# Kernel tuning notes

Measured on AMD Instinct MI355X. Metric: run time of the kernel, lower is better.

The kernel has to match this reference:

```python
import jax, jax.numpy as jnp
import numpy as np

B, N_VIS = 2, 512
T, HP, WP = 8, 16, 16
L = T * HP * WP              # 2048 tokens
D, HEAD_DIM = 384, 48
N_HEADS = D // HEAD_DIM      # 8
N_LAYERS, F_DIM = 8, 1536
EPS = 1e-6
THETA = 10000.0


def _rms(x, w):
    return x * jax.lax.rsqrt(jnp.mean(x * x, axis=-1, keepdims=True) + EPS) * w


def _rope_cos_sin(t, h, w):
    # VideoRotaryEmbeddingSplit466: split head_dim//2 freqs 4:6:6 over (t,h,w)
    half = HEAD_DIM // 2
    inv = 1.0 / (THETA ** (jnp.arange(half, dtype=jnp.float32) / half))
    dt = half * 4 // 16
    dh = half * 6 // 16
    l = jnp.arange(t * h * w)
    tp = l // (h * w)
    rem = l % (h * w)
    hp = rem // w
    wp = rem % w
    f = jnp.concatenate([tp[:, None] * inv[:dt],
                         hp[:, None] * inv[dt:dt + dh],
                         wp[:, None] * inv[dt + dh:]], axis=1)   # (L, half)
    emb = jnp.concatenate([f, f], axis=-1)                        # (L, HEAD_DIM)
    return jnp.cos(emb), jnp.sin(emb)


def _rot_half(x):
    x1, x2 = jnp.split(x, 2, axis=-1)
    return jnp.concatenate([-x2, x1], axis=-1)


def _forward(visible_embeddings, ids_restore, mask, t_frames, h_patches, w_patches,
             mask_token, ln_in_w, ln1_w, ln2_w, Wq, bq, Wk, bk, Wv, bv, Wo, bo,
             W1, b1, W2, b2):
    b, n_vis, d = visible_embeddings.shape
    l_full = ids_restore.shape[1]
    ppf = h_patches * w_patches
    n_mask = l_full - n_vis
    # append learnable mask tokens and un-shuffle with ids_restore
    x_cat = jnp.concatenate(
        [visible_embeddings, jnp.broadcast_to(mask_token, (b, n_mask, d))], axis=1)
    x_full = jnp.take_along_axis(x_cat, ids_restore[:, :, None].astype(jnp.int32), axis=1)
    # 3D RoPE over full grid
    cos, sin = _rope_cos_sin(t_frames, h_patches, w_patches)      # (L, HEAD_DIM)
    # frame-level mask, True = forbid. Faithful to torch broadcasting:
    # forbid[i, j] = frame_ids[j] < frame_ids[i]
    fid = jnp.arange(l_full) // ppf
    forbid = fid[None, :] < fid[:, None]                          # (L, L)
    bias = jnp.where(forbid, jnp.finfo(jnp.float32).min, 0.0)
    # pre-norm transformer stack (RMSNorm, exact GELU MLP)
    x = _rms(x_full, ln_in_w)
    scale = 1.0 / jnp.sqrt(jnp.float32(HEAD_DIM))
    cs = cos[None, :, None, :]
    sn = sin[None, :, None, :]
    for i in range(N_LAYERS):
        hdn = _rms(x, ln1_w[i])
        q = (hdn @ Wq[i] + bq[i]).reshape(b, l_full, N_HEADS, HEAD_DIM)
        k = (hdn @ Wk[i] + bk[i]).reshape(b, l_full, N_HEADS, HEAD_DIM)
        v = (hdn @ Wv[i] + bv[i]).reshape(b, l_full, N_HEADS, HEAD_DIM)
        q = q * cs + _rot_half(q) * sn
        k = k * cs + _rot_half(k) * sn
        s = jnp.einsum('bqhd,bkhd->bhqk', q, k) * scale + bias
        a = jax.nn.softmax(s, axis=-1)
        o = jnp.einsum('bhqk,bkhd->bqhd', a, v).reshape(b, l_full, d)
        x = x + o @ Wo[i] + bo[i]
        h2 = _rms(x, ln2_w[i])
        x = x + jax.nn.gelu(h2 @ W1[i] + b1[i], approximate=False) @ W2[i] + b2[i]
    decoded_full = x  # feature_head = Identity (feature_proj_dim is None)
    # split visible / masked: every row has exactly n_vis ones -> static shapes
    order = jnp.argsort(-mask, axis=1, stable=True)               # visible first, in order
    decoded_visible = jnp.take_along_axis(decoded_full, order[:, :n_vis, None], axis=1)
    decoded_masked = jnp.take_along_axis(decoded_full, order[:, n_vis:, None], axis=1)
    return decoded_full, decoded_visible, decoded_masked


def setup_inputs():
    key = jax.random.key(0)
    ks = jax.random.split(key, 12)
    vis = jax.random.normal(ks[0], (B, N_VIS, D), jnp.float32)
    noise = jax.random.uniform(ks[1], (B, L))
    ids_shuffle = jnp.argsort(noise, axis=1)
    ids_restore = jnp.argsort(ids_shuffle, axis=1).astype(jnp.int32)
    mask = jnp.zeros((B, L), jnp.int32).at[
        jnp.arange(B)[:, None], ids_shuffle[:, :N_VIS]].set(1)    # 1 = visible

    def p(k, shape):
        return jax.random.normal(k, shape, jnp.float32) * 0.02

    return {
        'visible_embeddings': vis, 'ids_restore': ids_restore, 'mask': mask,
        't_frames': T, 'h_patches': HP, 'w_patches': WP,
        'mask_token': p(ks[2], (D,)),
        'ln_in_w': jnp.ones((D,), jnp.float32),
        'ln1_w': jnp.ones((N_LAYERS, D), jnp.float32),
        'ln2_w': jnp.ones((N_LAYERS, D), jnp.float32),
        'Wq': p(ks[3], (N_LAYERS, D, D)), 'bq': jnp.zeros((N_LAYERS, D)),
        'Wk': p(ks[4], (N_LAYERS, D, D)), 'bk': jnp.zeros((N_LAYERS, D)),
        'Wv': p(ks[5], (N_LAYERS, D, D)), 'bv': jnp.zeros((N_LAYERS, D)),
        'Wo': p(ks[6], (N_LAYERS, D, D)), 'bo': jnp.zeros((N_LAYERS, D)),
        'W1': p(ks[7], (N_LAYERS, D, F_DIM)), 'b1': jnp.zeros((N_LAYERS, F_DIM)),
        'W2': p(ks[8], (N_LAYERS, F_DIM, D)), 'b2': jnp.zeros((N_LAYERS, D)),
    }


def reference(visible_embeddings, ids_restore, mask, t_frames, h_patches, w_patches,
              mask_token, ln_in_w, ln1_w, ln2_w, Wq, bq, Wk, bk, Wv, bv, Wo, bo,
              W1, b1, W2, b2):
    return _forward(visible_embeddings, ids_restore, mask, t_frames, h_patches,
                    w_patches, mask_token, ln_in_w, ln1_w, ln2_w, Wq, bq, Wk, bk,
                    Wv, bv, Wo, bo, W1, b1, W2, b2)
```

## Files before the change

kernel.cpp:

```cpp
#include <hip/hip_runtime.h>

typedef __attribute__((ext_vector_type(8))) __bf16 bf16x8;
typedef __attribute__((ext_vector_type(8))) unsigned short ushort8;
typedef __attribute__((ext_vector_type(4))) float floatx4;

#define NB 2
#define SEQ 2048
#define DIM 384
#define NH 8
#define HD 48
#define HDP 64
#define FF 1536
#define NLAYER 8
#define ATT_SCALE 0.14433756729740643f

__device__ __forceinline__ unsigned short f2bf(float f) {
  unsigned u = __builtin_bit_cast(unsigned, f);
  u += 0x7fffu + ((u >> 16) & 1u);
  return (unsigned short)(u >> 16);
}
__device__ __forceinline__ float bf2f(unsigned short h) {
  unsigned u = ((unsigned)h) << 16;
  return __builtin_bit_cast(float, u);
}
__device__ __forceinline__ bf16x8 ldb8(const unsigned short* p) {
  return __builtin_bit_cast(bf16x8, *(const ushort8*)p);
}
__device__ __forceinline__ void gl2lds16(const unsigned short* g, unsigned short* l) {
  __builtin_amdgcn_global_load_lds((const __attribute__((address_space(1))) unsigned int*)g,
                                   (__attribute__((address_space(3))) unsigned int*)l, 16, 0, 0);
}
#define MFMA(a, b, c) __builtin_amdgcn_mfma_f32_16x16x32_bf16(a, b, c, 0, 0, 0)

__global__ __launch_bounds__(256) void wtrans_kernel(const float* __restrict__ W,
                                                     unsigned short* __restrict__ Wt,
                                                     int K, int N,
                                                     size_t sstride, size_t dstride) {
  __shared__ unsigned short tile[32][33];
  const float* Wl = W + (size_t)blockIdx.z * sstride;
  unsigned short* Wtl = Wt + (size_t)blockIdx.z * dstride;
  int n0 = blockIdx.x * 32, k0 = blockIdx.y * 32;
  int tx = threadIdx.x, ty = threadIdx.y;
  for (int i = ty; i < 32; i += 8)
    tile[i][tx] = f2bf(Wl[(size_t)(k0 + i) * N + n0 + tx]);
  __syncthreads();
  for (int i = ty; i < 32; i += 8)
    Wtl[(size_t)(n0 + i) * K + k0 + tx] = tile[tx][i];
}

__global__ void biascat_kernel(const float* __restrict__ bq, const float* __restrict__ bk,
                               const float* __restrict__ bv, float* __restrict__ out) {
  int idx = blockIdx.x * 256 + threadIdx.x;
  if (idx >= NLAYER * 1152) return;
  int z = idx / 1152, j = idx % 1152;
  float v = (j < 384) ? bq[z * 384 + j] : (j < 768) ? bk[z * 384 + j - 384] : bv[z * 384 + j - 768];
  out[idx] = v;
}

__global__ void ropetab_kernel(float* __restrict__ cosT, float* __restrict__ sinT) {
  int idx = blockIdx.x * 256 + threadIdx.x;
  if (idx >= SEQ * HD) return;
  int l = idx / HD, d = idx % HD;
  int j = d % 24;
  float inv = powf(10000.0f, -(float)j / 24.0f);
  float pos;
  if (j < 6) pos = (float)(l >> 8);
  else if (j < 15) pos = (float)((l >> 4) & 15);
  else pos = (float)(l & 15);
  float f = pos * inv;
  cosT[idx] = cosf(f);
  sinT[idx] = sinf(f);
}

__global__ __launch_bounds__(256) void gatherrms_kernel(const float* __restrict__ vis,
                                                        const int* __restrict__ ids,
                                                        const float* __restrict__ mask_token,
                                                        const float* __restrict__ w,
                                                        float* __restrict__ x) {
  int wv = threadIdx.x >> 6, lane = threadIdx.x & 63;
  int row = blockIdx.x * 4 + wv;
  int b = row >> 11;
  int src = ids[row];
  const float* p = (src < 512) ? (vis + ((size_t)b * 512 + src) * DIM) : mask_token;
  float v[6];
  float ss = 0.f;
#pragma unroll
  for (int j = 0; j < 6; j++) { v[j] = p[lane + 64 * j]; ss += v[j] * v[j]; }
#pragma unroll
  for (int m = 32; m; m >>= 1) ss += __shfl_xor(ss, m);
  float s = rsqrtf(ss * (1.0f / DIM) + 1e-6f);
#pragma unroll
  for (int j = 0; j < 6; j++)
    x[(size_t)row * DIM + lane + 64 * j] = v[j] * s * w[lane + 64 * j];
}

__global__ __launch_bounds__(256) void rmsadd_kernel(float* __restrict__ x,
                                                     const float* __restrict__ p0,
                                                     const float* __restrict__ p1,
                                                     const float* __restrict__ w,
                                                     unsigned short* __restrict__ out,
                                                     int doadd) {
  int wv = threadIdx.x >> 6, lane = threadIdx.x & 63;
  int row = blockIdx.x * 4 + wv;
  size_t base = (size_t)row * DIM;
  float v[6];
  float ss = 0.f;
  if (doadd) {
#pragma unroll
    for (int j = 0; j < 6; j++) {
      int o = lane + 64 * j;
      v[j] = x[base + o] + p0[base + o] + p1[base + o];
      x[base + o] = v[j];
      ss += v[j] * v[j];
    }
  } else {
#pragma unroll
    for (int j = 0; j < 6; j++) { v[j] = x[base + lane + 64 * j]; ss += v[j] * v[j]; }
  }
#pragma unroll
  for (int m = 32; m; m >>= 1) ss += __shfl_xor(ss, m);
  float s = rsqrtf(ss * (1.0f / DIM) + 1e-6f);
#pragma unroll
  for (int j = 0; j < 6; j++)
    out[base + lane + 64 * j] = f2bf(v[j] * s * w[lane + 64 * j]);
}

__global__ __launch_bounds__(256) void gemm64_kernel(const unsigned short* __restrict__ A,
                                                     const unsigned short* __restrict__ Wt,
                                                     const float* __restrict__ bias,
                                                     int M, int N, int K, int mode,
                                                     unsigned short* __restrict__ outb,
                                                     unsigned short* __restrict__ outb2,
                                                     unsigned short* __restrict__ outv,
                                                     float* __restrict__ outf0,
                                                     float* __restrict__ outf1) {
  __shared__ __align__(16) unsigned short As[64 * 32];
  __shared__ __align__(16) unsigned short Bs[64 * 32];
  int tid = threadIdx.x;
  int wv = tid >> 6, lane = tid & 63;
  int wm = wv >> 1, wn = wv & 1;
  int row0 = blockIdx.x * 64, col0 = blockIdx.y * 64;
  int q = lane >> 4, c = lane & 15;
  int kchunk = K / gridDim.z;
  int kb0 = blockIdx.z * kchunk;
  floatx4 acc[2][2] = {};
  int sr = tid >> 2, sk = (tid & 3) * 8;
  const unsigned short* Ag = A + (size_t)(row0 + sr) * K + kb0 + sk;
  const unsigned short* Bg = Wt + (size_t)(col0 + sr) * K + kb0 + sk;
  unsigned short* Asl = As + tid * 8;
  unsigned short* Bsl = Bs + tid * 8;
  for (int k0 = 0; k0 < kchunk; k0 += 32) {
    gl2lds16(Ag + k0, Asl);
    gl2lds16(Bg + k0, Bsl);
    __syncthreads();
    bf16x8 a0 = ldb8(&As[(wm * 32 + c) * 32 + q * 8]);
    bf16x8 a1 = ldb8(&As[(wm * 32 + 16 + c) * 32 + q * 8]);
    bf16x8 b0 = ldb8(&Bs[(wn * 32 + c) * 32 + q * 8]);
    bf16x8 b1 = ldb8(&Bs[(wn * 32 + 16 + c) * 32 + q * 8]);
    acc[0][0] = MFMA(a0, b0, acc[0][0]);
    acc[0][1] = MFMA(a0, b1, acc[0][1]);
    acc[1][0] = MFMA(a1, b0, acc[1][0]);
    acc[1][1] = MFMA(a1, b1, acc[1][1]);
    __syncthreads();
  }
  float* outf = blockIdx.z ? outf1 : outf0;
  int addb = (blockIdx.z == 0);
#pragma unroll
  for (int tm = 0; tm < 2; tm++)
#pragma unroll
    for (int tn = 0; tn < 2; tn++)
#pragma unroll
      for (int r = 0; r < 4; r++) {
        int rg = row0 + wm * 32 + tm * 16 + q * 4 + r;
        int cg = col0 + wn * 32 + tn * 16 + c;
        float v = acc[tm][tn][r] + (addb ? bias[cg] : 0.f);
        if (mode == 3) {
          float g = v * 0.5f * (1.0f + erff(v * 0.70710678f));
          outb[(size_t)rg * N + cg] = f2bf(g);
        } else if (mode == 4) {
          if (cg < 384) {
            outb[(size_t)rg * 384 + cg] = f2bf(v);
          } else if (cg < 768) {
            outb2[(size_t)rg * 384 + cg - 384] = f2bf(v);
          } else {
            int j = cg - 768;
            int h = j / HD, hd = j % HD;
            int b = rg >> 11, l = rg & 2047;
            outv[(((size_t)b * NH + h) * HDP + hd) * SEQ + l] = f2bf(v);
          }
        } else {
          outf[(size_t)rg * N + cg] = v;
        }
      }
}

__global__ __launch_bounds__(384) void rope_kernel(const unsigned short* __restrict__ qpre,
                                                   const unsigned short* __restrict__ kpre,
                                                   const float* __restrict__ cosT,
                                                   const float* __restrict__ sinT,
                                                   unsigned short* __restrict__ qdst,
                                                   unsigned short* __restrict__ kdst) {
  int row = blockIdx.x;
  int b = row >> 11, l = row & 2047;
  int t = threadIdx.x;
  const unsigned short* src = (t >= 192) ? kpre : qpre;
  unsigned short* dst = (t >= 192) ? kdst : qdst;
  float sc = (t >= 192) ? 1.0f : ATT_SCALE;
  int pp = t % 192;
  int h = pp / 24, d = pp % 24;
  float x1 = bf2f(src[(size_t)row * DIM + h * HD + d]);
  float x2 = bf2f(src[(size_t)row * DIM + h * HD + d + 24]);
  float cs = cosT[l * HD + d], sn = sinT[l * HD + d];
  size_t base = (((size_t)b * NH + h) * SEQ + l) * HDP;
  dst[base + d] = f2bf((x1 * cs - x2 * sn) * sc);
  dst[base + d + 24] = f2bf((x2 * cs + x1 * sn) * sc);
}

__global__ __launch_bounds__(256) void fattn_kernel(const unsigned short* __restrict__ qb,
                                                    const unsigned short* __restrict__ kb,
                                                    const unsigned short* __restrict__ vt,
                                                    float* __restrict__ pO,
                                                    float* __restrict__ pM,
                                                    float* __restrict__ pL) {
  __shared__ __align__(16) unsigned short Ks[2][64][72];
  __shared__ __align__(16) unsigned short Vs[2][48][72];
  __shared__ __align__(16) unsigned short Pt[4][16][64];
  int tid = threadIdx.x;
  int wv = tid >> 6, lane = tid & 63;
  int q = lane >> 4, c = lane & 15;
  int i = blockIdx.x;
  int bh = 2 * (i & 7) + ((i >> 3) & 1);
  int rest = i >> 4;
  int z = rest & 1;
  int q0 = (rest >> 1) * 64;
  int kstart = q0 & ~255;
  int n = (SEQ - kstart) >> 6;
  int n2 = (n + 1) >> 1;
  int it0 = z * n2;
  int it1 = z ? n : n2;
  const unsigned short* qbase = qb + (size_t)bh * SEQ * HDP;
  const unsigned short* kbase = kb + (size_t)bh * SEQ * HDP;
  const unsigned short* vbase = vt + (size_t)bh * HDP * SEQ;
  int myrow = q0 + wv * 16;
  bf16x8 a0 = ldb8(qbase + (size_t)(myrow + c) * HDP + q * 8);
  bf16x8 a1 = ldb8(qbase + (size_t)(myrow + c) * HDP + 32 + q * 8);
  floatx4 O[3] = {};
  float mr[4] = {-3e38f, -3e38f, -3e38f, -3e38f};
  float lr[4] = {0.f, 0.f, 0.f, 0.f};
  int srow = tid >> 2, sch = (tid & 3) * 16;
  ushort8 kA, kB, vA, vB;
  const unsigned short* kg0 = kbase + (size_t)srow * HDP + sch;
  const unsigned short* vg0 = vbase + (size_t)srow * SEQ + sch;
  {
    int k0 = kstart + it0 * 64;
    kA = *(const ushort8*)(kg0 + (size_t)k0 * HDP);
    kB = *(const ushort8*)(kg0 + (size_t)k0 * HDP + 8);
    if (srow < 48) {
      vA = *(const ushort8*)(vg0 + k0);
      vB = *(const ushort8*)(vg0 + k0 + 8);
    }
  }
  for (int it = it0; it < it1; ++it) {
    int buf = it & 1;
    *(ushort8*)(&Ks[buf][srow][sch]) = kA;
    *(ushort8*)(&Ks[buf][srow][sch + 8]) = kB;
    if (srow < 48) {
      *(ushort8*)(&Vs[buf][srow][sch]) = vA;
      *(ushort8*)(&Vs[buf][srow][sch + 8]) = vB;
    }
    if (it + 1 < it1) {
      int k0 = kstart + (it + 1) * 64;
      kA = *(const ushort8*)(kg0 + (size_t)k0 * HDP);
      kB = *(const ushort8*)(kg0 + (size_t)k0 * HDP + 8);
      if (srow < 48) {
        vA = *(const ushort8*)(vg0 + k0);
        vB = *(const ushort8*)(vg0 + k0 + 8);
      }
    }
    __syncthreads();
    floatx4 S[4];
#pragma unroll
    for (int t = 0; t < 4; t++) {
      bf16x8 b0 = ldb8(&Ks[buf][t * 16 + c][q * 8]);
      bf16x8 b1 = ldb8(&Ks[buf][t * 16 + c][32 + q * 8]);
      floatx4 zz = {};
      zz = MFMA(a0, b0, zz);
      S[t] = MFMA(a1, b1, zz);
    }
    float alpha[4];
#pragma unroll
    for (int r = 0; r < 4; r++) {
      float m0 = fmaxf(fmaxf(S[0][r], S[1][r]), fmaxf(S[2][r], S[3][r]));
#pragma unroll
      for (int msk = 1; msk < 16; msk <<= 1) m0 = fmaxf(m0, __shfl_xor(m0, msk, 16));
      float nm = fmaxf(mr[r], m0);
      alpha[r] = __expf(mr[r] - nm);
      mr[r] = nm;
      lr[r] *= alpha[r];
    }
#pragma unroll
    for (int t = 0; t < 4; t++)
#pragma unroll
      for (int r = 0; r < 4; r++) {
        float pv = __expf(S[t][r] - mr[r]);
        lr[r] += pv;
        Pt[wv][q * 4 + r][t * 16 + c] = f2bf(pv);
      }
#pragma unroll
    for (int f = 0; f < 3; f++)
#pragma unroll
      for (int r = 0; r < 4; r++) O[f][r] *= alpha[r];
    bf16x8 pa0 = ldb8(&Pt[wv][c][q * 8]);
    bf16x8 pa1 = ldb8(&Pt[wv][c][32 + q * 8]);
#pragma unroll
    for (int f = 0; f < 3; f++) {
      bf16x8 v0 = ldb8(&Vs[buf][f * 16 + c][q * 8]);
      bf16x8 v1 = ldb8(&Vs[buf][f * 16 + c][32 + q * 8]);
      O[f] = MFMA(pa0, v0, O[f]);
      O[f] = MFMA(pa1, v1, O[f]);
    }
  }
#pragma unroll
  for (int r = 0; r < 4; r++)
#pragma unroll
    for (int msk = 1; msk < 16; msk <<= 1) lr[r] += __shfl_xor(lr[r], msk, 16);
  size_t pbase = (size_t)z * (NB * NH * SEQ) + (size_t)bh * SEQ + myrow;
#pragma unroll
  for (int r = 0; r < 4; r++) {
    int row = q * 4 + r;
    if (c == 0) {
      pM[pbase + row] = mr[r];
      pL[pbase + row] = lr[r];
    }
#pragma unroll
    for (int f = 0; f < 3; f++) pO[(pbase + row) * 48 + f * 16 + c] = O[f][r];
  }
}

__global__ __launch_bounds__(256) void amerge_kernel(const float* __restrict__ pO,
                                                     const float* __restrict__ pM,
                                                     const float* __restrict__ pL,
                                                     unsigned short* __restrict__ obuf) {
  int idx = blockIdx.x * 256 + threadIdx.x;
  int rowg = idx / 48, d = idx - rowg * 48;
  const int NR = NB * NH * SEQ;
  float m0 = pM[rowg], m1 = pM[NR + rowg];
  float l0 = pL[rowg], l1 = pL[NR + rowg];
  float M = fmaxf(m0, m1);
  float e0 = __expf(m0 - M), e1 = __expf(m1 - M);
  float inv = 1.0f / (l0 * e0 + l1 * e1);
  float v = (pO[(size_t)rowg * 48 + d] * e0 + pO[(size_t)(NR + rowg) * 48 + d] * e1) * inv;
  int bh = rowg >> 11, l = rowg & 2047;
  obuf[(((size_t)(bh >> 3)) * SEQ + l) * DIM + (bh & 7) * HD + d] = f2bf(v);
}

__global__ __launch_bounds__(256) void rank_kernel(const int* __restrict__ mask,
                                                   int* __restrict__ dest) {
  __shared__ int wsum[4];
  int b = blockIdx.x, t = threadIdx.x;
  int lane = t & 63, wv = t >> 6;
  const int* mb = mask + b * SEQ;
  int base = t * 8;
  int v[8];
  int s = 0;
#pragma unroll
  for (int j = 0; j < 8; j++) { v[j] = mb[base + j]; s += v[j]; }
  int incl = s;
  for (int off = 1; off < 64; off <<= 1) {
    int n = __shfl_up(incl, off);
    if (lane >= off) incl += n;
  }
  if (lane == 63) wsum[wv] = incl;
  __syncthreads();
  int P = incl - s;
  for (int w = 0; w < wv; w++) P += wsum[w];
  int run = 0;
#pragma unroll
  for (int j = 0; j < 8; j++) {
    int ones = P + run;
    int l = base + j;
    dest[b * SEQ + l] = v[j] ? ones : 512 + (l - ones);
    run += v[j];
  }
}

__global__ __launch_bounds__(256) void output_kernel(const float* __restrict__ x,
                                                     const float* __restrict__ p0,
                                                     const float* __restrict__ p1,
                                                     const int* __restrict__ dest,
                                                     float* __restrict__ out) {
  int idx = blockIdx.x * 256 + threadIdx.x;
  int row = idx / 96, c = idx % 96;
  size_t base_i = (size_t)row * DIM;
  float4 v = ((const float4*)(x + base_i))[c];
  float4 a = ((const float4*)(p0 + base_i))[c];
  float4 bb = ((const float4*)(p1 + base_i))[c];
  v.x += a.x + bb.x; v.y += a.y + bb.y; v.z += a.z + bb.z; v.w += a.w + bb.w;
  ((float4*)(out + base_i))[c] = v;
  int b = row >> 11;
  int d = dest[row];
  size_t base = (size_t)NB * SEQ * DIM;
  size_t o;
  if (d < 512) o = base + ((size_t)b * 512 + d) * DIM;
  else o = base + (size_t)NB * 512 * DIM + ((size_t)b * 1536 + (d - 512)) * DIM;
  ((float4*)(out + o))[c] = v;
}

extern "C" void kernel_launch(void* const* d_in, const int* in_sizes, int n_in,
                              void* d_out, int out_size, void* d_ws, size_t ws_size,
                              hipStream_t stream) {
  const float* vis = (const float*)d_in[0];
  const int* ids = (const int*)d_in[1];
  const int* mask = (const int*)d_in[2];
  const float* mask_token = (const float*)d_in[6];
  const float* ln_in_w = (const float*)d_in[7];
  const float* ln1_w = (const float*)d_in[8];
  const float* ln2_w = (const float*)d_in[9];
  const float* Wq = (const float*)d_in[10];
  const float* bq = (const float*)d_in[11];
  const float* Wk = (const float*)d_in[12];
  const float* bk = (const float*)d_in[13];
  const float* Wv = (const float*)d_in[14];
  const float* bv = (const float*)d_in[15];
  const float* Wo = (const float*)d_in[16];
  const float* bo = (const float*)d_in[17];
  const float* W1 = (const float*)d_in[18];
  const float* b1 = (const float*)d_in[19];
  const float* W2 = (const float*)d_in[20];
  const float* b2 = (const float*)d_in[21];

  char* p = (char*)d_ws;
  size_t off = 0;
  auto alloc = [&](size_t n) -> void* {
    off = (off + 255) & ~(size_t)255;
    void* r = p + off;
    off += n;
    return r;
  };
  unsigned short* wqkvT = (unsigned short*)alloc((size_t)NLAYER * 1152 * DIM * 2);
  unsigned short* woT = (unsigned short*)alloc((size_t)NLAYER * DIM * DIM * 2);
  unsigned short* w1T = (unsigned short*)alloc((size_t)NLAYER * DIM * FF * 2);
  unsigned short* w2T = (unsigned short*)alloc((size_t)NLAYER * DIM * FF * 2);
  float* bqkv = (float*)alloc((size_t)NLAYER * 1152 * 4);
  float* cosT = (float*)alloc((size_t)SEQ * HD * 4);
  float* sinT = (float*)alloc((size_t)SEQ * HD * 4);
  float* x = (float*)alloc((size_t)NB * SEQ * DIM * 4);
  unsigned short* hdn = (unsigned short*)alloc((size_t)NB * SEQ * DIM * 2);
  unsigned short* qpre = (unsigned short*)alloc((size_t)NB * SEQ * DIM * 2);
  unsigned short* kpre = (unsigned short*)alloc((size_t)NB * SEQ * DIM * 2);
  unsigned short* qb = (unsigned short*)alloc((size_t)NB * NH * SEQ * HDP * 2);
  unsigned short* kb = (unsigned short*)alloc((size_t)NB * NH * SEQ * HDP * 2);
  unsigned short* vtb = (unsigned short*)alloc((size_t)NB * NH * SEQ * HDP * 2);
  unsigned short* obuf = (unsigned short*)alloc((size_t)NB * SEQ * DIM * 2);
  unsigned short* a1 = (unsigned short*)alloc((size_t)NB * SEQ * FF * 2);
  float* pA0 = (float*)alloc((size_t)NB * SEQ * DIM * 4);
  float* pA1 = (float*)alloc((size_t)NB * SEQ * DIM * 4);
  float* pB0 = (float*)alloc((size_t)NB * SEQ * DIM * 4);
  float* pB1 = (float*)alloc((size_t)NB * SEQ * DIM * 4);
  float* pO = (float*)alloc((size_t)2 * NB * NH * SEQ * 48 * 4);
  float* pM = (float*)alloc((size_t)2 * NB * NH * SEQ * 4);
  float* pL = (float*)alloc((size_t)2 * NB * NH * SEQ * 4);
  int* dest = (int*)alloc((size_t)NB * SEQ * 4);

  hipMemsetAsync(qb, 0, (size_t)NB * NH * SEQ * HDP * 2, stream);
  hipMemsetAsync(kb, 0, (size_t)NB * NH * SEQ * HDP * 2, stream);

  dim3 tb(32, 8);
  wtrans_kernel<<<dim3(12, 12, 8), tb, 0, stream>>>(Wq, wqkvT, 384, 384, 147456, 442368);
  wtrans_kernel<<<dim3(12, 12, 8), tb, 0, stream>>>(Wk, wqkvT + 147456, 384, 384, 147456, 442368);
  wtrans_kernel<<<dim3(12, 12, 8), tb, 0, stream>>>(Wv, wqkvT + 294912, 384, 384, 147456, 442368);
  wtrans_kernel<<<dim3(12, 12, 8), tb, 0, stream>>>(Wo, woT, 384, 384, 147456, 147456);
  wtrans_kernel<<<dim3(48, 12, 8), tb, 0, stream>>>(W1, w1T, 384, 1536, 589824, 589824);
  wtrans_kernel<<<dim3(12, 48, 8), tb, 0, stream>>>(W2, w2T, 1536, 384, 589824, 589824);
  biascat_kernel<<<(NLAYER * 1152 + 255) / 256, 256, 0, stream>>>(bq, bk, bv, bqkv);
  ropetab_kernel<<<(SEQ * HD + 255) / 256, 256, 0, stream>>>(cosT, sinT);
  gatherrms_kernel<<<NB * SEQ / 4, 256, 0, stream>>>(vis, ids, mask_token, ln_in_w, x);

  for (int i = 0; i < NLAYER; i++) {
    size_t wo = (size_t)i * DIM * DIM;
    size_t wf = (size_t)i * DIM * FF;
    rmsadd_kernel<<<NB * SEQ / 4, 256, 0, stream>>>(x, pB0, pB1, ln1_w + i * DIM, hdn, i > 0);
    gemm64_kernel<<<dim3(64, 18, 1), 256, 0, stream>>>(hdn, wqkvT + (size_t)i * 442368,
                                                       bqkv + i * 1152, NB * SEQ, 1152, DIM, 4,
                                                       qpre, kpre, vtb, nullptr, nullptr);
    rope_kernel<<<NB * SEQ, 384, 0, stream>>>(qpre, kpre, cosT, sinT, qb, kb);
    fattn_kernel<<<1024, 256, 0, stream>>>(qb, kb, vtb, pO, pM, pL);
    amerge_kernel<<<NB * NH * SEQ * 48 / 256, 256, 0, stream>>>(pO, pM, pL, obuf);
    gemm64_kernel<<<dim3(64, 6, 2), 256, 0, stream>>>(obuf, woT + wo, bo + i * DIM, NB * SEQ, DIM,
                                                      DIM, 5, nullptr, nullptr, nullptr, pA0, pA1);
    rmsadd_kernel<<<NB * SEQ / 4, 256, 0, stream>>>(x, pA0, pA1, ln2_w + i * DIM, hdn, 1);
    gemm64_kernel<<<dim3(64, 24, 1), 256, 0, stream>>>(hdn, w1T + wf, b1 + i * FF, NB * SEQ, FF,
                                                       DIM, 3, a1, nullptr, nullptr, nullptr,
                                                       nullptr);
    gemm64_kernel<<<dim3(64, 6, 2), 256, 0, stream>>>(a1, w2T + wf, b2 + i * DIM, NB * SEQ, DIM,
                                                      FF, 5, nullptr, nullptr, nullptr, pB0, pB1);
  }
  rank_kernel<<<NB, 256, 0, stream>>>(mask, dest);
  output_kernel<<<NB * SEQ * 96 / 256, 256, 0, stream>>>(x, pB0, pB1, dest, (float*)d_out);
}
```

Baseline: 1.053 ms.

## Fuse RoPE into QKV GEMM epilogue and attention merge into output projection

Q/K weight columns are permuted at setup so RoPE pairs sit in adjacent lanes, which lets the QKV GEMM epilogue apply the rotation with a lane shuffle and write head-major Q/K directly. This removes the separate rope kernel and the qpre/kpre round trip. The split-KV attention merge is now done while loading A tiles in the Wo GEMM, which removes the amerge kernel and the obuf buffer. GEMMs become templated, and some use a K step of 64 to halve barriers per K step; the fused A-load adds scalar fp32 loads and exp work inside the GEMM main loop.

Result: faster. 935.7 us (-11.1%).

```diff
diff --git a/kernel.cpp b/kernel.cpp
--- a/kernel.cpp
+++ b/kernel.cpp
@@ -12,6 +12,7 @@
 #define HDP 64
 #define FF 1536
 #define NLAYER 8
+#define NRG (NB * NH * SEQ)
 #define ATT_SCALE 0.14433756729740643f
 
 __device__ __forceinline__ unsigned short f2bf(float f) {
@@ -34,8 +35,8 @@
 
 __global__ __launch_bounds__(256) void wtrans_kernel(const float* __restrict__ W,
                                                      unsigned short* __restrict__ Wt,
-                                                     int K, int N,
-                                                     size_t sstride, size_t dstride) {
+                                                     int K, int N, size_t sstride, size_t dstride,
+                                                     int permqk) {
   __shared__ unsigned short tile[32][33];
   const float* Wl = W + (size_t)blockIdx.z * sstride;
   unsigned short* Wtl = Wt + (size_t)blockIdx.z * dstride;
@@ -44,8 +45,14 @@
   for (int i = ty; i < 32; i += 8)
     tile[i][tx] = f2bf(Wl[(size_t)(k0 + i) * N + n0 + tx]);
   __syncthreads();
-  for (int i = ty; i < 32; i += 8)
-    Wtl[(size_t)(n0 + i) * K + k0 + tx] = tile[tx][i];
+  for (int i = ty; i < 32; i += 8) {
+    int n = n0 + i;
+    if (permqk) {
+      int h = n / 48, d = n % 48;
+      n = h * 48 + (d < 24 ? 2 * d : 2 * (d - 24) + 1);
+    }
+    Wtl[(size_t)n * K + k0 + tx] = tile[tx][i];
+  }
 }
 
 __global__ void biascat_kernel(const float* __restrict__ bq, const float* __restrict__ bk,
@@ -53,23 +60,27 @@
   int idx = blockIdx.x * 256 + threadIdx.x;
   if (idx >= NLAYER * 1152) return;
   int z = idx / 1152, j = idx % 1152;
-  float v = (j < 384) ? bq[z * 384 + j] : (j < 768) ? bk[z * 384 + j - 384] : bv[z * 384 + j - 768];
-  out[idx] = v;
-}
-
-__global__ void ropetab_kernel(float* __restrict__ cosT, float* __restrict__ sinT) {
+  int part = j / 384, jj = j % 384;
+  float v = (part == 0) ? bq[z * 384 + jj] : (part == 1) ? bk[z * 384 + jj] : bv[z * 384 + jj];
+  int dst = j;
+  if (part < 2) {
+    int h = jj / 48, d = jj % 48;
+    dst = part * 384 + h * 48 + (d < 24 ? 2 * d : 2 * (d - 24) + 1);
+  }
+  out[z * 1152 + dst] = v;
+}
+
+__global__ void ropetab_kernel(float2* __restrict__ cs2) {
   int idx = blockIdx.x * 256 + threadIdx.x;
-  if (idx >= SEQ * HD) return;
-  int l = idx / HD, d = idx % HD;
-  int j = d % 24;
-  float inv = powf(10000.0f, -(float)j / 24.0f);
+  if (idx >= SEQ * 24) return;
+  int l = idx / 24, f = idx % 24;
+  float inv = powf(10000.0f, -(float)f / 24.0f);
   float pos;
-  if (j < 6) pos = (float)(l >> 8);
-  else if (j < 15) pos = (float)((l >> 4) & 15);
+  if (f < 6) pos = (float)(l >> 8);
+  else if (f < 15) pos = (float)((l >> 4) & 15);
   else pos = (float)(l & 15);
-  float f = pos * inv;
-  cosT[idx] = cosf(f);
-  sinT[idx] = sinf(f);
+  float ang = pos * inv;
+  cs2[idx] = make_float2(cosf(ang), sinf(ang));
 }
 
 __global__ __launch_bounds__(256) void gatherrms_kernel(const float* __restrict__ vis,
@@ -125,17 +136,21 @@
     out[base + lane + 64 * j] = f2bf(v[j] * s * w[lane + 64 * j]);
 }
 
+template <int KSTEP, int MODE>
 __global__ __launch_bounds__(256) void gemm64_kernel(const unsigned short* __restrict__ A,
                                                      const unsigned short* __restrict__ Wt,
-                                                     const float* __restrict__ bias,
-                                                     int M, int N, int K, int mode,
+                                                     const float* __restrict__ bias, int N, int K,
                                                      unsigned short* __restrict__ outb,
                                                      unsigned short* __restrict__ outb2,
                                                      unsigned short* __restrict__ outv,
                                                      float* __restrict__ outf0,
-                                                     float* __restrict__ outf1) {
-  __shared__ __align__(16) unsigned short As[64 * 32];
-  __shared__ __align__(16) unsigned short Bs[64 * 32];
+                                                     float* __restrict__ outf1,
+                                                     const float* __restrict__ pO,
+                                                     const float* __restrict__ pM,
+                                                     const float* __restrict__ pL,
+                                                     const float2* __restrict__ cs2) {
+  __shared__ __align__(16) unsigned short As[64 * KSTEP];
+  __shared__ __align__(16) unsigned short Bs[64 * KSTEP];
   int tid = threadIdx.x;
   int wv = tid >> 6, lane = tid & 63;
   int wm = wv >> 1, wn = wv & 1;
@@ -149,19 +164,89 @@
   const unsigned short* Bg = Wt + (size_t)(col0 + sr) * K + kb0 + sk;
   unsigned short* Asl = As + tid * 8;
   unsigned short* Bsl = Bs + tid * 8;
-  for (int k0 = 0; k0 < kchunk; k0 += 32) {
-    gl2lds16(Ag + k0, Asl);
-    gl2lds16(Bg + k0, Bsl);
+  for (int k0 = 0; k0 < kchunk; k0 += KSTEP) {
+    if (MODE == 6) {
+      int row = row0 + sr, b = row >> 11, l = row & 2047;
+      int kc = kb0 + k0 + sk;
+      int h = kc / 48, d0 = kc % 48;
+      int rowg = (b * 8 + h) * SEQ + l;
+      float m0 = pM[rowg], m1 = pM[NRG + rowg];
+      float l0 = pL[rowg], l1 = pL[NRG + rowg];
+      float M = fmaxf(m0, m1);
+      float e0 = __expf(m0 - M), e1 = __expf(m1 - M);
+      float inv = 1.0f / (l0 * e0 + l1 * e1);
+      e0 *= inv;
+      e1 *= inv;
+      const float* P0 = pO + (size_t)rowg * 48 + d0;
+      const float* P1 = pO + ((size_t)NRG + rowg) * 48 + d0;
+      ushort8 av;
+#pragma unroll
+      for (int j = 0; j < 8; j++) av[j] = f2bf(P0[j] * e0 + P1[j] * e1);
+      *(ushort8*)Asl = av;
+      gl2lds16(Bg + k0, Bsl);
+    } else if (KSTEP == 32) {
+      gl2lds16(Ag + k0, Asl);
+      gl2lds16(Bg + k0, Bsl);
+    } else {
+      gl2lds16(Ag + k0, Asl);
+      gl2lds16(Ag + k0 + 32, Asl + 2048);
+      gl2lds16(Bg + k0, Bsl);
+      gl2lds16(Bg + k0 + 32, Bsl + 2048);
+    }
     __syncthreads();
-    bf16x8 a0 = ldb8(&As[(wm * 32 + c) * 32 + q * 8]);
-    bf16x8 a1 = ldb8(&As[(wm * 32 + 16 + c) * 32 + q * 8]);
-    bf16x8 b0 = ldb8(&Bs[(wn * 32 + c) * 32 + q * 8]);
-    bf16x8 b1 = ldb8(&Bs[(wn * 32 + 16 + c) * 32 + q * 8]);
-    acc[0][0] = MFMA(a0, b0, acc[0][0]);
-    acc[0][1] = MFMA(a0, b1, acc[0][1]);
-    acc[1][0] = MFMA(a1, b0, acc[1][0]);
-    acc[1][1] = MFMA(a1, b1, acc[1][1]);
+    if (KSTEP == 32 || MODE == 6) {
+      bf16x8 a0 = ldb8(&As[(wm * 32 + c) * 32 + q * 8]);
+      bf16x8 a1 = ldb8(&As[(wm * 32 + 16 + c) * 32 + q * 8]);
+      bf16x8 b0 = ldb8(&Bs[(wn * 32 + c) * 32 + q * 8]);
+      bf16x8 b1 = ldb8(&Bs[(wn * 32 + 16 + c) * 32 + q * 8]);
+      acc[0][0] = MFMA(a0, b0, acc[0][0]);
+      acc[0][1] = MFMA(a0, b1, acc[0][1]);
+      acc[1][0] = MFMA(a1, b0, acc[1][0]);
+      acc[1][1] = MFMA(a1, b1, acc[1][1]);
+    } else {
+      bf16x8 aA[2], aB[2], bA[2], bB[2];
+#pragma unroll
+      for (int mt = 0; mt < 2; mt++) {
+        aA[mt] = ldb8(&As[(wm * 32 + mt * 16 + c) * 32 + q * 8]);
+        aB[mt] = ldb8(&As[2048 + (wm * 32 + mt * 16 + c) * 32 + q * 8]);
+      }
+#pragma unroll
+      for (int nt = 0; nt < 2; nt++) {
+        bA[nt] = ldb8(&Bs[(wn * 32 + nt * 16 + c) * 32 + q * 8]);
+        bB[nt] = ldb8(&Bs[2048 + (wn * 32 + nt * 16 + c) * 32 + q * 8]);
+      }
+#pragma unroll
+      for (int mt = 0; mt < 2; mt++)
+#pragma unroll
+        for (int nt = 0; nt < 2; nt++) {
+          acc[mt][nt] = MFMA(aA[mt], bA[nt], acc[mt][nt]);
+          acc[mt][nt] = MFMA(aB[mt], bB[nt], acc[mt][nt]);
+        }
+    }
     __syncthreads();
+  }
+  if (MODE == 4 && col0 < 768) {
+    const int isq = (col0 < 384) ? 1 : 0;
+    unsigned short* dst = isq ? outb : outb2;
+    float sc = isq ? ATT_SCALE : 1.0f;
+#pragma unroll
+    for (int tm = 0; tm < 2; tm++)
+#pragma unroll
+      for (int tn = 0; tn < 2; tn++)
+#pragma unroll
+        for (int r = 0; r < 4; r++) {
+          int rg = row0 + wm * 32 + tm * 16 + q * 4 + r;
+          int cg = col0 + wn * 32 + tn * 16 + c;
+          float v = acc[tm][tn][r] + bias[cg];
+          float pv = __shfl_xor(v, 1);
+          int cl = isq ? cg : cg - 384;
+          int h = cl / 48, s = cl % 48;
+          int l = rg & 2047, b = rg >> 11;
+          float2 cs = cs2[l * 24 + (s >> 1)];
+          float o = v * cs.x + ((s & 1) ? pv * cs.y : -pv * cs.y);
+          dst[(((size_t)(b * 8 + h)) * SEQ + l) * HDP + s] = f2bf(o * sc);
+        }
+    return;
   }
   float* outf = blockIdx.z ? outf1 : outf0;
   int addb = (blockIdx.z == 0);
@@ -174,46 +259,18 @@
         int rg = row0 + wm * 32 + tm * 16 + q * 4 + r;
         int cg = col0 + wn * 32 + tn * 16 + c;
         float v = acc[tm][tn][r] + (addb ? bias[cg] : 0.f);
-        if (mode == 3) {
+        if (MODE == 3) {
           float g = v * 0.5f * (1.0f + erff(v * 0.70710678f));
           outb[(size_t)rg * N + cg] = f2bf(g);
-        } else if (mode == 4) {
-          if (cg < 384) {
-            outb[(size_t)rg * 384 + cg] = f2bf(v);
-          } else if (cg < 768) {
-            outb2[(size_t)rg * 384 + cg - 384] = f2bf(v);
-          } else {
-            int j = cg - 768;
-            int h = j / HD, hd = j % HD;
-            int b = rg >> 11, l = rg & 2047;
-            outv[(((size_t)b * NH + h) * HDP + hd) * SEQ + l] = f2bf(v);
-          }
+        } else if (MODE == 4) {
+          int j = cg - 768;
+          int h = j / HD, hd = j % HD;
+          int b = rg >> 11, l = rg & 2047;
+          outv[(((size_t)b * NH + h) * HDP + hd) * SEQ + l] = f2bf(v);
         } else {
           outf[(size_t)rg * N + cg] = v;
         }
       }
-}
-
-__global__ __launch_bounds__(384) void rope_kernel(const unsigned short* __restrict__ qpre,
-                                                   const unsigned short* __restrict__ kpre,
-                                                   const float* __restrict__ cosT,
-                                                   const float* __restrict__ sinT,
-                                                   unsigned short* __restrict__ qdst,
-                                                   unsigned short* __restrict__ kdst) {
-  int row = blockIdx.x;
-  int b = row >> 11, l = row & 2047;
-  int t = threadIdx.x;
-  const unsigned short* src = (t >= 192) ? kpre : qpre;
-  unsigned short* dst = (t >= 192) ? kdst : qdst;
-  float sc = (t >= 192) ? 1.0f : ATT_SCALE;
-  int pp = t % 192;
-  int h = pp / 24, d = pp % 24;
-  float x1 = bf2f(src[(size_t)row * DIM + h * HD + d]);
-  float x2 = bf2f(src[(size_t)row * DIM + h * HD + d + 24]);
-  float cs = cosT[l * HD + d], sn = sinT[l * HD + d];
-  size_t base = (((size_t)b * NH + h) * SEQ + l) * HDP;
-  dst[base + d] = f2bf((x1 * cs - x2 * sn) * sc);
-  dst[base + d + 24] = f2bf((x2 * cs + x1 * sn) * sc);
 }
 
 __global__ __launch_bounds__(256) void fattn_kernel(const unsigned short* __restrict__ qb,
@@ -324,7 +381,7 @@
   for (int r = 0; r < 4; r++)
 #pragma unroll
     for (int msk = 1; msk < 16; msk <<= 1) lr[r] += __shfl_xor(lr[r], msk, 16);
-  size_t pbase = (size_t)z * (NB * NH * SEQ) + (size_t)bh * SEQ + myrow;
+  size_t pbase = (size_t)z * NRG + (size_t)bh * SEQ + myrow;
 #pragma unroll
   for (int r = 0; r < 4; r++) {
     int row = q * 4 + r;
@@ -335,23 +392,6 @@
 #pragma unroll
     for (int f = 0; f < 3; f++) pO[(pbase + row) * 48 + f * 16 + c] = O[f][r];
   }
-}
-
-__global__ __launch_bounds__(256) void amerge_kernel(const float* __restrict__ pO,
-                                                     const float* __restrict__ pM,
-                                                     const float* __restrict__ pL,
-                                                     unsigned short* __restrict__ obuf) {
-  int idx = blockIdx.x * 256 + threadIdx.x;
-  int rowg = idx / 48, d = idx - rowg * 48;
-  const int NR = NB * NH * SEQ;
-  float m0 = pM[rowg], m1 = pM[NR + rowg];
-  float l0 = pL[rowg], l1 = pL[NR + rowg];
-  float M = fmaxf(m0, m1);
-  float e0 = __expf(m0 - M), e1 = __expf(m1 - M);
-  float inv = 1.0f / (l0 * e0 + l1 * e1);
-  float v = (pO[(size_t)rowg * 48 + d] * e0 + pO[(size_t)(NR + rowg) * 48 + d] * e1) * inv;
-  int bh = rowg >> 11, l = rowg & 2047;
-  obuf[(((size_t)(bh >> 3)) * SEQ + l) * DIM + (bh & 7) * HD + d] = f2bf(v);
 }
 
 __global__ __launch_bounds__(256) void rank_kernel(const int* __restrict__ mask,
@@ -442,58 +482,53 @@
   unsigned short* w1T = (unsigned short*)alloc((size_t)NLAYER * DIM * FF * 2);
   unsigned short* w2T = (unsigned short*)alloc((size_t)NLAYER * DIM * FF * 2);
   float* bqkv = (float*)alloc((size_t)NLAYER * 1152 * 4);
-  float* cosT = (float*)alloc((size_t)SEQ * HD * 4);
-  float* sinT = (float*)alloc((size_t)SEQ * HD * 4);
+  float2* cs2 = (float2*)alloc((size_t)SEQ * 24 * 8);
   float* x = (float*)alloc((size_t)NB * SEQ * DIM * 4);
   unsigned short* hdn = (unsigned short*)alloc((size_t)NB * SEQ * DIM * 2);
-  unsigned short* qpre = (unsigned short*)alloc((size_t)NB * SEQ * DIM * 2);
-  unsigned short* kpre = (unsigned short*)alloc((size_t)NB * SEQ * DIM * 2);
   unsigned short* qb = (unsigned short*)alloc((size_t)NB * NH * SEQ * HDP * 2);
   unsigned short* kb = (unsigned short*)alloc((size_t)NB * NH * SEQ * HDP * 2);
   unsigned short* vtb = (unsigned short*)alloc((size_t)NB * NH * SEQ * HDP * 2);
-  unsigned short* obuf = (unsigned short*)alloc((size_t)NB * SEQ * DIM * 2);
   unsigned short* a1 = (unsigned short*)alloc((size_t)NB * SEQ * FF * 2);
   float* pA0 = (float*)alloc((size_t)NB * SEQ * DIM * 4);
   float* pA1 = (float*)alloc((size_t)NB * SEQ * DIM * 4);
   float* pB0 = (float*)alloc((size_t)NB * SEQ * DIM * 4);
   float* pB1 = (float*)alloc((size_t)NB * SEQ * DIM * 4);
-  float* pO = (float*)alloc((size_t)2 * NB * NH * SEQ * 48 * 4);
-  float* pM = (float*)alloc((size_t)2 * NB * NH * SEQ * 4);
-  float* pL = (float*)alloc((size_t)2 * NB * NH * SEQ * 4);
+  float* pO = (float*)alloc((size_t)2 * NRG * 48 * 4);
+  float* pM = (float*)alloc((size_t)2 * NRG * 4);
+  float* pL = (float*)alloc((size_t)2 * NRG * 4);
   int* dest = (int*)alloc((size_t)NB * SEQ * 4);
 
-  hipMemsetAsync(qb, 0, (size_t)NB * NH * SEQ * HDP * 2, stream);
-  hipMemsetAsync(kb, 0, (size_t)NB * NH * SEQ * HDP * 2, stream);
+  hipMemsetAsync(qb, 0, (size_t)2 * NB * NH * SEQ * HDP * 2, stream);
 
   dim3 tb(32, 8);
-  wtrans_kernel<<<dim3(12, 12, 8), tb, 0, stream>>>(Wq, wqkvT, 384, 384, 147456, 442368);
-  wtrans_kernel<<<dim3(12, 12, 8), tb, 0, stream>>>(Wk, wqkvT + 147456, 384, 384, 147456, 442368);
-  wtrans_kernel<<<dim3(12, 12, 8), tb, 0, stream>>>(Wv, wqkvT + 294912, 384, 384, 147456, 442368);
-  wtrans_kernel<<<dim3(12, 12, 8), tb, 0, stream>>>(Wo, woT, 384, 384, 147456, 147456);
-  wtrans_kernel<<<dim3(48, 12, 8), tb, 0, stream>>>(W1, w1T, 384, 1536, 589824, 589824);
-  wtrans_kernel<<<dim3(12, 48, 8), tb, 0, stream>>>(W2, w2T, 1536, 384, 589824, 589824);
+  wtrans_kernel<<<dim3(12, 12, 8), tb, 0, stream>>>(Wq, wqkvT, 384, 384, 147456, 442368, 1);
+  wtrans_kernel<<<dim3(12, 12, 8), tb, 0, stream>>>(Wk, wqkvT + 147456, 384, 384, 147456, 442368, 1);
+  wtrans_kernel<<<dim3(12, 12, 8), tb, 0, stream>>>(Wv, wqkvT + 294912, 384, 384, 147456, 442368, 0);
+  wtrans_kernel<<<dim3(12, 12, 8), tb, 0, stream>>>(Wo, woT, 384, 384, 147456, 147456, 0);
+  wtrans_kernel<<<dim3(48, 12, 8), tb, 0, stream>>>(W1, w1T, 384, 1536, 589824, 589824, 0);
+  wtrans_kernel<<<dim3(12, 48, 8), tb, 0, stream>>>(W2, w2T, 1536, 384, 589824, 589824, 0);
   biascat_kernel<<<(NLAYER * 1152 + 255) / 256, 256, 0, stream>>>(bq, bk, bv, bqkv);
-  ropetab_kernel<<<(SEQ * HD + 255) / 256, 256, 0, stream>>>(cosT, sinT);
+  ropetab_kernel<<<(SEQ * 24 + 255) / 256, 256, 0, stream>>>(cs2);
   gatherrms_kernel<<<NB * SEQ / 4, 256, 0, stream>>>(vis, ids, mask_token, ln_in_w, x);
 
   for (int i = 0; i < NLAYER; i++) {
     size_t wo = (size_t)i * DIM * DIM;
     size_t wf = (size_t)i * DIM * FF;
     rmsadd_kernel<<<NB * SEQ / 4, 256, 0, stream>>>(x, pB0, pB1, ln1_w + i * DIM, hdn, i > 0);
-    gemm64_kernel<<<dim3(64, 18, 1), 256, 0, stream>>>(hdn, wqkvT + (size_t)i * 442368,
-                                                       bqkv + i * 1152, NB * SEQ, 1152, DIM, 4,
-                                                       qpre, kpre, vtb, nullptr, nullptr);
-    rope_kernel<<<NB * SEQ, 384, 0, stream>>>(qpre, kpre, cosT, sinT, qb, kb);
+    gemm64_kernel<64, 4><<<dim3(64, 18, 1), 256, 0, stream>>>(
+        hdn, wqkvT + (size_t)i * 442368, bqkv + i * 1152, 1152, DIM, qb, kb, vtb, nullptr, nullptr,
+        nullptr, nullptr, nullptr, cs2);
     fattn_kernel<<<1024, 256, 0, stream>>>(qb, kb, vtb, pO, pM, pL);
-    amerge_kernel<<<NB * NH * SEQ * 48 / 256, 256, 0, stream>>>(pO, pM, pL, obuf);
-    gemm64_kernel<<<dim3(64, 6, 2), 256, 0, stream>>>(obuf, woT + wo, bo + i * DIM, NB * SEQ, DIM,
-                                                      DIM, 5, nullptr, nullptr, nullptr, pA0, pA1);
+    gemm64_kernel<32, 6><<<dim3(64, 6, 2), 256, 0, stream>>>(
+        nullptr, woT + wo, bo + i * DIM, DIM, DIM, nullptr, nullptr, nullptr, pA0, pA1, pO, pM, pL,
+        nullptr);
     rmsadd_kernel<<<NB * SEQ / 4, 256, 0, stream>>>(x, pA0, pA1, ln2_w + i * DIM, hdn, 1);
-    gemm64_kernel<<<dim3(64, 24, 1), 256, 0, stream>>>(hdn, w1T + wf, b1 + i * FF, NB * SEQ, FF,
-                                                       DIM, 3, a1, nullptr, nullptr, nullptr,
-                                                       nullptr);
-    gemm64_kernel<<<dim3(64, 6, 2), 256, 0, stream>>>(a1, w2T + wf, b2 + i * DIM, NB * SEQ, DIM,
-                                                      FF, 5, nullptr, nullptr, nullptr, pB0, pB1);
+    gemm64_kernel<64, 3><<<dim3(64, 24, 1), 256, 0, stream>>>(
+        hdn, w1T + wf, b1 + i * FF, FF, DIM, a1, nullptr, nullptr, nullptr, nullptr, nullptr,
+        nullptr, nullptr, nullptr);
+    gemm64_kernel<64, 5><<<dim3(64, 6, 2), 256, 0, stream>>>(
+        a1, w2T + wf, b2 + i * DIM, DIM, FF, nullptr, nullptr, nullptr, pB0, pB1, nullptr, nullptr,
+        nullptr, nullptr);
   }
   rank_kernel<<<NB, 256, 0, stream>>>(mask, dest);
   output_kernel<<<NB * SEQ * 96 / 256, 256, 0, stream>>>(x, pB0, pB1, dest, (float*)d_out);
```
